# Performance work log

Measured on AMD Instinct MI355X. Metric: run time of the kernel, lower is better.

The kernel has to match this reference:

```python
import jax, jax.numpy as jnp
import numpy as np

EPS = 1e-12

def _l2norm(v, axis):
    n = jnp.sqrt(jnp.sum(v * v, axis=axis, keepdims=True))
    return v / jnp.maximum(n, EPS)

def setup_inputs() -> dict:
    key = jax.random.key(0)
    ks = jax.random.split(key, 6)
    b, m, C = 32, 8192, 512
    K, d = 8, C // 8  # num_cluster, reduced dims
    x = jax.random.normal(ks[0], (b, m, C), dtype=jnp.float32)
    mask = jnp.ones((b, m), dtype=bool)
    # reduction Linear: in_channels -> d
    W_red = jax.random.normal(ks[1], (d, C), dtype=jnp.float32) / np.sqrt(C)
    b_red = jax.random.normal(ks[2], (d,), dtype=jnp.float32) * 0.01
    # cluster assignment Linear: d -> K
    W_lin = jax.random.normal(ks[3], (K, d), dtype=jnp.float32) / np.sqrt(d)
    b_lin = jax.random.normal(ks[4], (K,), dtype=jnp.float32) * 0.01
    centroids = jax.random.uniform(ks[5], (K, d), dtype=jnp.float32)
    return {"x": x, "mask": mask, "W_red": W_red, "b_red": b_red,
            "W_lin": W_lin, "b_lin": b_lin, "centroids": centroids}

def reference(x, mask, W_red, b_red, W_lin, b_lin, centroids):
    # reduction: [b,m,C] -> [b,m,d]
    x = jnp.einsum('bmc,dc->bmd', x, W_red) + b_red
    # L2-normalize descriptors over feature dim (BaseAggregator.forward)
    x = _l2norm(x, axis=2)
    # soft assignment: [b,m,K]
    logits = jnp.einsum('bmd,kd->bmk', x, W_lin) + b_lin
    a = jax.nn.softmax(logits, axis=2)
    # VLAD: sum_m a[b,m,k] * (x[b,m,d] - c[k,d])
    #     = (a^T @ x) - c * sum_m a   -- avoids the b*m*k*d intermediate
    vlad = jnp.einsum('bmk,bmd->bkd', a, x) \
         - centroids[None] * jnp.sum(a, axis=1)[..., None]
    # intra-normalize per cluster, flatten, global L2-normalize
    vlad = _l2norm(vlad, axis=2)
    vlad = vlad.reshape(vlad.shape[0], -1)
    return _l2norm(vlad, axis=1)
```

## Files before the change

### kernel.cpp

```cpp
#include <hip/hip_runtime.h>
#include <hip/hip_bf16.h>

typedef __attribute__((ext_vector_type(8))) __bf16 bf16x8;
typedef __attribute__((ext_vector_type(4))) float f32x4;

#define NBATCH 32
#define MDIM 8192
#define CDIM 512
#define DDIM 64
#define KCLU 8
#define MT 128
#define KCH 32
#define ASTR 40
#define NT 80

static constexpr int ACC_OFF   = 0;
static constexpr int SUMA_OFF  = 16384;
static constexpr int DOTWB_OFF = 16640;
static constexpr size_t BHI_OFF = 66592;
static constexpr size_t BLO_OFF = BHI_OFF + (size_t)NT * CDIM * 2;

__device__ __forceinline__ unsigned short f32_bf16_rne(float x) {
  unsigned u = __float_as_uint(x);
  u += 0x7fffu + ((u >> 16) & 1u);
  return (unsigned short)(u >> 16);
}

__device__ __forceinline__ void split2(float v, unsigned short& h, unsigned short& l) {
  unsigned u = __float_as_uint(v);
  unsigned hu = u & 0xffff0000u;
  h = (unsigned short)(hu >> 16);
  l = f32_bf16_rne(v - __uint_as_float(hu));
}

__global__ void netvlad_prep(const float* __restrict__ W_red,
                             const float* __restrict__ b_red,
                             const float* __restrict__ W_lin,
                             const float* __restrict__ b_lin,
                             float* __restrict__ ws_f,
                             unsigned short* __restrict__ Bhi,
                             unsigned short* __restrict__ Blo) {
  int gid = blockIdx.x * 256 + threadIdx.x;
  if (gid < NT * CDIM) {
    int n = gid >> 9, cc = gid & 511;
    float v = 0.f;
    if (n < 64) {
      v = W_red[gid];
    } else if (n < 72) {
      int k = n - 64;
      float s = 0.f;
      for (int d = 0; d < 64; ++d) s += W_lin[k * 64 + d] * W_red[d * 512 + cc];
      v = s;
    }
    unsigned short h, l;
    split2(v, h, l);
    Bhi[gid] = h;
    Blo[gid] = l;
  } else if (gid < NT * CDIM + 16640) {
    ws_f[gid - NT * CDIM] = 0.f;
  } else if (gid < NT * CDIM + 16640 + 8) {
    int k = gid - (NT * CDIM + 16640);
    float s = 0.f;
    for (int d = 0; d < 64; ++d) s += W_lin[k * 64 + d] * b_red[d];
    ws_f[DOTWB_OFF + k] = s;
  }
}

__global__ __launch_bounds__(256, 3)
void netvlad_main(const float* __restrict__ x,
                  const float* __restrict__ b_red,
                  const float* __restrict__ b_lin,
                  float* __restrict__ ws_f,
                  const unsigned short* __restrict__ Bhi_g,
                  const unsigned short* __restrict__ Blo_g) {
  __shared__ unsigned short Ahi[MT * ASTR];
  __shared__ unsigned short Alo[MT * ASTR];
  __shared__ unsigned short Bhi[NT * ASTR];
  __shared__ unsigned short Blo[NT * ASTR];
  __shared__ float redv[4 * KCLU * DDIM];
  __shared__ float reds[4 * KCLU];

  const int tid = threadIdx.x;
  const int bb  = blockIdx.y;
  const int m0  = blockIdx.x * MT;
  const int w = tid >> 6;
  const int l = tid & 63;
  const int q = l >> 4;
  const int c = l & 15;

  f32x4 acc[2][5];
#pragma unroll
  for (int tm = 0; tm < 2; ++tm)
#pragma unroll
    for (int ct = 0; ct < 5; ++ct) acc[tm][ct] = (f32x4){0.f, 0.f, 0.f, 0.f};

  const float dw = (c < 8) ? ws_f[DOTWB_OFF + c] : 0.f;
  const float bl = (c < 8) ? b_lin[c] : 0.f;
  float bred[4];
#pragma unroll
  for (int ct = 0; ct < 4; ++ct) bred[ct] = b_red[ct * 16 + c];

  for (int kc = 0; kc < CDIM / KCH; ++kc) {
    __syncthreads();
    const int kbase = kc * KCH;
#pragma unroll
    for (int i = 0; i < 2; ++i) {
      const int id = tid + 256 * i;
      const int row = id >> 2, g = id & 3;
      const float* src = x + ((size_t)(bb * MDIM + m0 + row)) * CDIM + kbase + g * 8;
      f32x4 p0 = *(const f32x4*)src;
      f32x4 p1 = *(const f32x4*)(src + 4);
      float vv[8] = {p0[0], p0[1], p0[2], p0[3], p1[0], p1[1], p1[2], p1[3]};
      unsigned hp[4], lp[4];
#pragma unroll
      for (int j = 0; j < 4; ++j) {
        unsigned short h0, l0, h1, l1;
        split2(vv[2 * j], h0, l0);
        split2(vv[2 * j + 1], h1, l1);
        hp[j] = (unsigned)h0 | ((unsigned)h1 << 16);
        lp[j] = (unsigned)l0 | ((unsigned)l1 << 16);
      }
      uint4 hv; hv.x = hp[0]; hv.y = hp[1]; hv.z = hp[2]; hv.w = hp[3];
      uint4 lv; lv.x = lp[0]; lv.y = lp[1]; lv.z = lp[2]; lv.w = lp[3];
      *(uint4*)&Ahi[row * ASTR + g * 8] = hv;
      *(uint4*)&Alo[row * ASTR + g * 8] = lv;
    }
#pragma unroll
    for (int i = 0; i < 3; ++i) {
      const int id = tid + 256 * i;
      if (id < 640) {
        const int half = (id >= 320);
        const int id2 = id - half * 320;
        const int row = id2 >> 2, g = id2 & 3;
        const unsigned short* src = (half ? Blo_g : Bhi_g) + (size_t)row * CDIM + kbase + g * 8;
        uint4 p = *(const uint4*)src;
        unsigned short* dst = (half ? Blo : Bhi) + row * ASTR + g * 8;
        *(uint4*)dst = p;
      }
    }
    __syncthreads();
    bf16x8 ah[2], al_[2], bh[5], blv[5];
#pragma unroll
    for (int tm = 0; tm < 2; ++tm) {
      const int ro = (w * 32 + tm * 16 + c) * ASTR + q * 8;
      ah[tm]  = *(const bf16x8*)&Ahi[ro];
      al_[tm] = *(const bf16x8*)&Alo[ro];
    }
#pragma unroll
    for (int ct = 0; ct < 5; ++ct) {
      const int ro = (ct * 16 + c) * ASTR + q * 8;
      bh[ct]  = *(const bf16x8*)&Bhi[ro];
      blv[ct] = *(const bf16x8*)&Blo[ro];
    }
#pragma unroll
    for (int tm = 0; tm < 2; ++tm)
#pragma unroll
      for (int ct = 0; ct < 5; ++ct) {
        acc[tm][ct] = __builtin_amdgcn_mfma_f32_16x16x32_bf16(ah[tm],  bh[ct],  acc[tm][ct], 0, 0, 0);
        acc[tm][ct] = __builtin_amdgcn_mfma_f32_16x16x32_bf16(ah[tm],  blv[ct], acc[tm][ct], 0, 0, 0);
        acc[tm][ct] = __builtin_amdgcn_mfma_f32_16x16x32_bf16(al_[tm], bh[ct],  acc[tm][ct], 0, 0, 0);
      }
  }

  float va[8][4];
#pragma unroll
  for (int k = 0; k < 8; ++k)
#pragma unroll
    for (int j = 0; j < 4; ++j) va[k][j] = 0.f;
  float suma_l = 0.f;

#pragma unroll
  for (int tm = 0; tm < 2; ++tm) {
#pragma unroll
    for (int r = 0; r < 4; ++r) {
      float y0 = acc[tm][0][r] + bred[0];
      float y1 = acc[tm][1][r] + bred[1];
      float y2 = acc[tm][2][r] + bred[2];
      float y3 = acc[tm][3][r] + bred[3];
      float sq = y0 * y0 + y1 * y1 + y2 * y2 + y3 * y3;
      sq += __shfl_xor(sq, 1); sq += __shfl_xor(sq, 2);
      sq += __shfl_xor(sq, 4); sq += __shfl_xor(sq, 8);
      const float rinv = 1.0f / fmaxf(sqrtf(sq), 1e-12f);
      const float u  = acc[tm][4][r] + dw;
      const float lg = rinv * u + bl;
      float e = (c < 8) ? __expf(lg) : 0.f;
      float s = e;
      s += __shfl_xor(s, 1); s += __shfl_xor(s, 2); s += __shfl_xor(s, 4);
      const float a  = (c < 8) ? e / s : 0.f;
      suma_l += a;
      const float ae = a * rinv;
#pragma unroll
      for (int k = 0; k < 8; ++k) {
        const float aek = __shfl(ae, (l & 48) + k);
        va[k][0] += aek * y0; va[k][1] += aek * y1;
        va[k][2] += aek * y2; va[k][3] += aek * y3;
      }
    }
  }
#pragma unroll
  for (int k = 0; k < 8; ++k)
#pragma unroll
    for (int j = 0; j < 4; ++j) {
      va[k][j] += __shfl_xor(va[k][j], 16);
      va[k][j] += __shfl_xor(va[k][j], 32);
    }
  suma_l += __shfl_xor(suma_l, 16);
  suma_l += __shfl_xor(suma_l, 32);

  if (q == 0) {
#pragma unroll
    for (int k = 0; k < 8; ++k)
#pragma unroll
      for (int j = 0; j < 4; ++j)
        redv[(w * KCLU + k) * DDIM + j * 16 + c] = va[k][j];
    if (c < 8) reds[w * KCLU + c] = suma_l;
  }
  __syncthreads();
  for (int idx = tid; idx < KCLU * DDIM; idx += 256) {
    float v = redv[idx] + redv[KCLU * DDIM + idx] +
              redv[2 * KCLU * DDIM + idx] + redv[3 * KCLU * DDIM + idx];
    atomicAdd(&ws_f[ACC_OFF + bb * KCLU * DDIM + idx], v);
  }
  if (tid < KCLU) {
    float v = reds[tid] + reds[KCLU + tid] + reds[2 * KCLU + tid] + reds[3 * KCLU + tid];
    atomicAdd(&ws_f[SUMA_OFF + bb * KCLU + tid], v);
  }
}

__global__ void netvlad_finish(const float* __restrict__ ws_f,
                               const float* __restrict__ centroids,
                               float* __restrict__ out) {
  const int bb = blockIdx.x;
  const int t = threadIdx.x;
  const int k = t >> 6, d = t & 63;
  __shared__ float s8[8];
  const float suma = ws_f[SUMA_OFF + bb * KCLU + k];
  float v = ws_f[ACC_OFF + (bb * KCLU + k) * DDIM + d] - centroids[k * DDIM + d] * suma;
  float sq = v * v;
#pragma unroll
  for (int off = 1; off < 64; off <<= 1) sq += __shfl_xor(sq, off);
  const float rinv = 1.0f / fmaxf(sqrtf(sq), 1e-12f);
  const float vn = v * rinv;
  if (d == 0) s8[k] = sq * rinv * rinv;
  __syncthreads();
  float g = 0.f;
#pragma unroll
  for (int i = 0; i < 8; ++i) g += s8[i];
  const float gr = 1.0f / fmaxf(sqrtf(g), 1e-12f);
  out[bb * 512 + t] = vn * gr;
}

extern "C" void kernel_launch(void* const* d_in, const int* in_sizes, int n_in,
                              void* d_out, int out_size, void* d_ws, size_t ws_size,
                              hipStream_t stream) {
  const float* x         = (const float*)d_in[0];
  const float* W_red     = (const float*)d_in[2];
  const float* b_red     = (const float*)d_in[3];
  const float* W_lin     = (const float*)d_in[4];
  const float* b_lin     = (const float*)d_in[5];
  const float* centroids = (const float*)d_in[6];
  float* ws_f = (float*)d_ws;
  unsigned short* Bhi = (unsigned short*)((char*)d_ws + BHI_OFF);
  unsigned short* Blo = (unsigned short*)((char*)d_ws + BLO_OFF);
  float* out = (float*)d_out;

  int prep_tasks = NT * CDIM + 16640 + 8;
  netvlad_prep<<<(prep_tasks + 255) / 256, 256, 0, stream>>>(
      W_red, b_red, W_lin, b_lin, ws_f, Bhi, Blo);

  dim3 grid(MDIM / MT, NBATCH);
  netvlad_main<<<grid, 256, 0, stream>>>(x, b_red, b_lin, ws_f, Bhi, Blo);

  netvlad_finish<<<NBATCH, 512, 0, stream>>>(ws_f, centroids, out);
}
```

Measured before the change: 719.3 us.

## Load operands directly from global into MFMA registers, drop LDS staging and x lo-split

Removes the shared-memory staging of x and the weight matrices, so each lane loads its MFMA fragments straight from global memory and the per-chunk barriers go away. The A operand is now rounded to a single bf16 (RNE) instead of being split into hi/lo parts, which cuts the MFMA count per tile from three to two and drops the Alo work. In exchange, accuracy on x falls to bf16, global loads are less coalesced (each lane reads 32-byte pieces from rows strided by C), and the B fragments are re-read from global/L2 by every wave.

```diff
diff --git a/kernel.cpp b/kernel.cpp
--- a/kernel.cpp
+++ b/kernel.cpp
@@ -10,8 +10,6 @@
 #define DDIM 64
 #define KCLU 8
 #define MT 128
-#define KCH 32
-#define ASTR 40
 #define NT 80
 
 static constexpr int ACC_OFF   = 0;
@@ -66,6 +64,15 @@
   }
 }
 
+__device__ __forceinline__ bf16x8 cvt8_rne(const f32x4& p0, const f32x4& p1) {
+  union { unsigned u[4]; bf16x8 v; } r;
+  r.u[0] = (unsigned)f32_bf16_rne(p0[0]) | ((unsigned)f32_bf16_rne(p0[1]) << 16);
+  r.u[1] = (unsigned)f32_bf16_rne(p0[2]) | ((unsigned)f32_bf16_rne(p0[3]) << 16);
+  r.u[2] = (unsigned)f32_bf16_rne(p1[0]) | ((unsigned)f32_bf16_rne(p1[1]) << 16);
+  r.u[3] = (unsigned)f32_bf16_rne(p1[2]) | ((unsigned)f32_bf16_rne(p1[3]) << 16);
+  return r.v;
+}
+
 __global__ __launch_bounds__(256, 3)
 void netvlad_main(const float* __restrict__ x,
                   const float* __restrict__ b_red,
@@ -73,10 +80,6 @@
                   float* __restrict__ ws_f,
                   const unsigned short* __restrict__ Bhi_g,
                   const unsigned short* __restrict__ Blo_g) {
-  __shared__ unsigned short Ahi[MT * ASTR];
-  __shared__ unsigned short Alo[MT * ASTR];
-  __shared__ unsigned short Bhi[NT * ASTR];
-  __shared__ unsigned short Blo[NT * ASTR];
   __shared__ float redv[4 * KCLU * DDIM];
   __shared__ float reds[4 * KCLU];
 
@@ -100,67 +103,36 @@
 #pragma unroll
   for (int ct = 0; ct < 4; ++ct) bred[ct] = b_red[ct * 16 + c];
 
-  for (int kc = 0; kc < CDIM / KCH; ++kc) {
-    __syncthreads();
-    const int kbase = kc * KCH;
-#pragma unroll
-    for (int i = 0; i < 2; ++i) {
-      const int id = tid + 256 * i;
-      const int row = id >> 2, g = id & 3;
-      const float* src = x + ((size_t)(bb * MDIM + m0 + row)) * CDIM + kbase + g * 8;
-      f32x4 p0 = *(const f32x4*)src;
-      f32x4 p1 = *(const f32x4*)(src + 4);
-      float vv[8] = {p0[0], p0[1], p0[2], p0[3], p1[0], p1[1], p1[2], p1[3]};
-      unsigned hp[4], lp[4];
-#pragma unroll
-      for (int j = 0; j < 4; ++j) {
-        unsigned short h0, l0, h1, l1;
-        split2(vv[2 * j], h0, l0);
-        split2(vv[2 * j + 1], h1, l1);
-        hp[j] = (unsigned)h0 | ((unsigned)h1 << 16);
-        lp[j] = (unsigned)l0 | ((unsigned)l1 << 16);
-      }
-      uint4 hv; hv.x = hp[0]; hv.y = hp[1]; hv.z = hp[2]; hv.w = hp[3];
-      uint4 lv; lv.x = lp[0]; lv.y = lp[1]; lv.z = lp[2]; lv.w = lp[3];
-      *(uint4*)&Ahi[row * ASTR + g * 8] = hv;
-      *(uint4*)&Alo[row * ASTR + g * 8] = lv;
-    }
-#pragma unroll
-    for (int i = 0; i < 3; ++i) {
-      const int id = tid + 256 * i;
-      if (id < 640) {
-        const int half = (id >= 320);
-        const int id2 = id - half * 320;
-        const int row = id2 >> 2, g = id2 & 3;
-        const unsigned short* src = (half ? Blo_g : Bhi_g) + (size_t)row * CDIM + kbase + g * 8;
-        uint4 p = *(const uint4*)src;
-        unsigned short* dst = (half ? Blo : Bhi) + row * ASTR + g * 8;
-        *(uint4*)dst = p;
-      }
-    }
-    __syncthreads();
-    bf16x8 ah[2], al_[2], bh[5], blv[5];
-#pragma unroll
-    for (int tm = 0; tm < 2; ++tm) {
-      const int ro = (w * 32 + tm * 16 + c) * ASTR + q * 8;
-      ah[tm]  = *(const bf16x8*)&Ahi[ro];
-      al_[tm] = *(const bf16x8*)&Alo[ro];
-    }
+  const float* a0p = x + ((size_t)(bb * MDIM + m0 + w * 32 + c)) * CDIM + q * 8;
+  const float* a1p = a0p + 16 * CDIM;
+  const unsigned short* bp = (size_t)(c) * CDIM + q * 8 + (const unsigned short*)0 + 0;
+  const size_t boff = (size_t)c * CDIM + q * 8;
+
+#pragma unroll 2
+  for (int kc = 0; kc < CDIM / 32; ++kc) {
+    const int kb = kc * 32;
+    f32x4 a0lo = *(const f32x4*)(a0p + kb);
+    f32x4 a0hi = *(const f32x4*)(a0p + kb + 4);
+    f32x4 a1lo = *(const f32x4*)(a1p + kb);
+    f32x4 a1hi = *(const f32x4*)(a1p + kb + 4);
+    bf16x8 bh[5], blv[5];
 #pragma unroll
     for (int ct = 0; ct < 5; ++ct) {
-      const int ro = (ct * 16 + c) * ASTR + q * 8;
-      bh[ct]  = *(const bf16x8*)&Bhi[ro];
-      blv[ct] = *(const bf16x8*)&Blo[ro];
-    }
-#pragma unroll
-    for (int tm = 0; tm < 2; ++tm)
-#pragma unroll
-      for (int ct = 0; ct < 5; ++ct) {
-        acc[tm][ct] = __builtin_amdgcn_mfma_f32_16x16x32_bf16(ah[tm],  bh[ct],  acc[tm][ct], 0, 0, 0);
-        acc[tm][ct] = __builtin_amdgcn_mfma_f32_16x16x32_bf16(ah[tm],  blv[ct], acc[tm][ct], 0, 0, 0);
-        acc[tm][ct] = __builtin_amdgcn_mfma_f32_16x16x32_bf16(al_[tm], bh[ct],  acc[tm][ct], 0, 0, 0);
-      }
-  }
+      const size_t ro = boff + (size_t)(ct * 16) * CDIM + kb;
+      bh[ct]  = *(const bf16x8*)(Bhi_g + ro);
+      blv[ct] = *(const bf16x8*)(Blo_g + ro);
+    }
+    bf16x8 a0 = cvt8_rne(a0lo, a0hi);
+    bf16x8 a1 = cvt8_rne(a1lo, a1hi);
+#pragma unroll
+    for (int ct = 0; ct < 5; ++ct) {
+      acc[0][ct] = __builtin_amdgcn_mfma_f32_16x16x32_bf16(a0, bh[ct],  acc[0][ct], 0, 0, 0);
+      acc[0][ct] = __builtin_amdgcn_mfma_f32_16x16x32_bf16(a0, blv[ct], acc[0][ct], 0, 0, 0);
+      acc[1][ct] = __builtin_amdgcn_mfma_f32_16x16x32_bf16(a1, bh[ct],  acc[1][ct], 0, 0, 0);
+      acc[1][ct] = __builtin_amdgcn_mfma_f32_16x16x32_bf16(a1, blv[ct], acc[1][ct], 0, 0, 0);
+    }
+  }
+  (void)bp;
 
   float va[8][4];
 #pragma unroll
```

Measured after the change: 852.6 us. 18.5% more time.
